# Performance work log

Measured on AMD Instinct MI355X. Metric: run time of the kernel, lower is better.

Reference implementation:

```python
import jax, jax.numpy as jnp
import numpy as np

N_AST = 400_000   # number of AST nodes
M_MAP = 400_000   # number of (ast_node -> cfg_node) mapping entries
S_CFG = 100_000   # number of CFG (PDG) nodes
D = 256           # ast_node_encoding_dim
H = 8             # attention heads
HD = D // H       # head dim
OUT = 256         # combined_dim


def setup_inputs() -> dict:
    key = jax.random.key(0)
    ks = jax.random.split(key, 12)
    w = lambda k, shp: (jax.random.normal(k, shp, jnp.float32) * 0.02)
    return {
        "ast_nodes_encodings": jax.random.normal(ks[0], (N_AST, D), jnp.float32),
        "W_q": w(ks[1], (D, D)), "b_q": jnp.zeros((D,), jnp.float32),
        "W_k": w(ks[2], (D, D)), "b_k": jnp.zeros((D,), jnp.float32),
        "W_v": w(ks[3], (D, D)), "b_v": jnp.zeros((D,), jnp.float32),
        "W_o": w(ks[4], (D, OUT)), "b_o": jnp.zeros((OUT,), jnp.float32),
        "ast_node_idx_to_pdg_node_idx_mapping_key": jax.random.randint(ks[5], (M_MAP,), 0, N_AST),
        "ast_node_idx_to_pdg_node_idx_mapping_value": jax.random.randint(ks[6], (M_MAP,), 0, S_CFG),
        "pdg_node_idx_to_sub_ast_root_idx_mapping_key": jnp.arange(S_CFG),
        "pdg_node_idx_to_sub_ast_root_idx_mapping_value": jax.random.randint(ks[7], (S_CFG,), 0, N_AST),
        "nr_cfg_nodes": S_CFG,
    }


def reference(ast_nodes_encodings, W_q, b_q, W_k, b_k, W_v, b_v, W_o, b_o,
              ast_node_idx_to_pdg_node_idx_mapping_key,
              ast_node_idx_to_pdg_node_idx_mapping_value,
              pdg_node_idx_to_sub_ast_root_idx_mapping_key,
              pdg_node_idx_to_sub_ast_root_idx_mapping_value,
              nr_cfg_nodes):
    S = int(nr_cfg_nodes)
    D_ = ast_nodes_encodings.shape[1]

    # Build per-CFG-node attention queries: gather sub-AST root encodings then
    # scatter into a [S, D] zero buffer (keys are a bijection -> .set is exact).
    gathered_q = ast_nodes_encodings[pdg_node_idx_to_sub_ast_root_idx_mapping_value]  # [S, D]
    attn_queries = jnp.zeros((S, D_), ast_nodes_encodings.dtype).at[
        pdg_node_idx_to_sub_ast_root_idx_mapping_key].set(gathered_q)

    # Scattered inputs: one row per (ast node -> cfg node) mapping entry.
    x = ast_nodes_encodings[ast_node_idx_to_pdg_node_idx_mapping_key]  # [M, D]
    idx = ast_node_idx_to_pdg_node_idx_mapping_value                   # [M] segment ids
    M = x.shape[0]

    # Multi-head projections.
    q = (attn_queries @ W_q + b_q).reshape(S, H, HD)  # [S, H, HD]
    k = (x @ W_k + b_k).reshape(M, H, HD)             # [M, H, HD]
    v = (x @ W_v + b_v).reshape(M, H, HD)             # [M, H, HD]

    # Per-element, per-head attention logits against the owning segment's query.
    scale = np.float32(1.0 / np.sqrt(HD))
    scores = jnp.einsum('mhd,mhd->mh', k, q[idx]) * scale  # [M, H]

    # Segment-wise (scatter) softmax, numerically stable.
    seg_max = jax.ops.segment_max(scores, idx, num_segments=S)        # [S, H]
    seg_max = jnp.where(jnp.isfinite(seg_max), seg_max, jnp.zeros_like(seg_max))
    ew = jnp.exp(scores - seg_max[idx])                               # [M, H]
    denom = jax.ops.segment_sum(ew, idx, num_segments=S)              # [S, H]
    pooled = jax.ops.segment_sum(ew[:, :, None] * v, idx, num_segments=S)  # [S, H, HD]
    pooled = pooled / jnp.maximum(denom, 1e-9)[:, :, None]

    # Output projection to combined_dim.
    out = pooled.reshape(S, H * HD) @ W_o + b_o  # [S, OUT]
    return out
```

## Files before the change

kernel.cpp:

```cpp
#include <hip/hip_runtime.h>
#include <hip/hip_bf16.h>


typedef __attribute__((ext_vector_type(8))) short bf16x8;
typedef __attribute__((ext_vector_type(4))) float f32x4;

#define DEV __device__ __forceinline__

DEV float bf2f(unsigned short u) {
    union { unsigned int i; float f; } x;
    x.i = ((unsigned int)u) << 16;
    return x.f;
}

DEV unsigned short f2bf(float f) {
    union { float f; unsigned int i; } x;
    x.f = f;
    unsigned int i = x.i;
    unsigned int r = 0x7fffu + ((i >> 16) & 1u);
    return (unsigned short)((i + r) >> 16);
}

DEV bf16x8 cvt8(float4 lo, float4 hi) {
    union { bf16x8 v; unsigned int u[4]; } r;
    asm("v_cvt_pk_bf16_f32 %0, %1, %2" : "=v"(r.u[0]) : "v"(lo.x), "v"(lo.y));
    asm("v_cvt_pk_bf16_f32 %0, %1, %2" : "=v"(r.u[1]) : "v"(lo.z), "v"(lo.w));
    asm("v_cvt_pk_bf16_f32 %0, %1, %2" : "=v"(r.u[2]) : "v"(hi.x), "v"(hi.y));
    asm("v_cvt_pk_bf16_f32 %0, %1, %2" : "=v"(r.u[3]) : "v"(hi.z), "v"(hi.w));
    return r.v;
}

DEV unsigned int pack2(float a, float b) {
    unsigned int r;
    asm("v_cvt_pk_bf16_f32 %0, %1, %2" : "=v"(r) : "v"(a), "v"(b));
    return r;
}

DEV int swz(int row, int c) {
    return row * 256 + ((((c) >> 3) ^ (row & 7)) << 3);
}

__global__ void convert_weights(const float* __restrict__ Wq,
                                const float* __restrict__ Wk,
                                const float* __restrict__ Wv,
                                const float* __restrict__ Wo,
                                const float* __restrict__ bk,
                                const float* __restrict__ bv,
                                unsigned short* __restrict__ Wtq,
                                unsigned short* __restrict__ Wtkv,
                                unsigned short* __restrict__ Wto,
                                float* __restrict__ bkv) {
    int t = blockIdx.x * 256 + threadIdx.x;
    if (t < 65536) {
        int n = t >> 8, k = t & 255;
        Wtq[t] = f2bf(Wq[k * 256 + n]);
    } else if (t < 65536 + 131072) {
        int u = t - 65536;
        int n = u >> 8, k = u & 255;
        Wtkv[u] = f2bf(n < 256 ? Wk[k * 256 + n] : Wv[k * 256 + (n - 256)]);
    } else if (t < 196608 + 65536) {
        int u = t - 196608;
        int n = u >> 8, k = u & 255;
        Wto[u] = f2bf(Wo[k * 256 + n]);
    } else if (t < 262144 + 512) {
        int c = t - 262144;
        bkv[c] = c < 256 ? bk[c] : bv[c - 256];
    }
}

__global__ void zero_kernel(int* __restrict__ p, int n) {
    int i = blockIdx.x * 256 + threadIdx.x;
    if (i < n) p[i] = 0;
}

__global__ void hist_kernel(const int* __restrict__ map_val,
                            int* __restrict__ counts, int M) {
    int m = blockIdx.x * 256 + threadIdx.x;
    if (m < M) atomicAdd(&counts[map_val[m]], 1);
}

__global__ __launch_bounds__(256) void scan_p1(const int* __restrict__ counts,
                                               int* __restrict__ bsum, int S) {
    const int i = blockIdx.x * 256 + threadIdx.x;
    int v = (i < S) ? counts[i] : 0;
#pragma unroll
    for (int d = 1; d < 64; d <<= 1) v += __shfl_xor(v, d);
    __shared__ int ws[4];
    if ((threadIdx.x & 63) == 0) ws[threadIdx.x >> 6] = v;
    __syncthreads();
    if (threadIdx.x == 0) bsum[blockIdx.x] = ws[0] + ws[1] + ws[2] + ws[3];
}

__global__ __launch_bounds__(256) void scan_p2(const int* __restrict__ bsum,
                                               int* __restrict__ bpref,
                                               int* __restrict__ offsets,
                                               int nb, int S) {
    __shared__ int part[256];
    const int t = threadIdx.x;
    const int chunk = (nb + 255) / 256;
    const int lo = t * chunk;
    const int hi = min(lo + chunk, nb);
    int sum = 0;
    for (int i = lo; i < hi; ++i) sum += bsum[i];
    part[t] = sum;
    __syncthreads();
    for (int d = 1; d < 256; d <<= 1) {
        int v = (t >= d) ? part[t - d] : 0;
        __syncthreads();
        part[t] += v;
        __syncthreads();
    }
    int run = (t > 0) ? part[t - 1] : 0;
    for (int i = lo; i < hi; ++i) {
        bpref[i] = run;
        run += bsum[i];
    }
    if (t == 255) offsets[S] = part[255];
}

__global__ __launch_bounds__(256) void scan_p3(const int* __restrict__ counts,
                                               const int* __restrict__ bpref,
                                               int* __restrict__ offsets,
                                               int* __restrict__ cursor, int S) {
    __shared__ int sh[256];
    const int t = threadIdx.x;
    const int i = blockIdx.x * 256 + t;
    const int v = (i < S) ? counts[i] : 0;
    sh[t] = v;
    __syncthreads();
    for (int d = 1; d < 256; d <<= 1) {
        int u = (t >= d) ? sh[t - d] : 0;
        __syncthreads();
        sh[t] += u;
        __syncthreads();
    }
    if (i < S) {
        const int e = sh[t] - v + bpref[blockIdx.x];
        offsets[i] = e;
        cursor[i] = e;
    }
}

__global__ void scatter_kernel(const int* __restrict__ map_key,
                               const int* __restrict__ map_val,
                               int* __restrict__ cursor,
                               int* __restrict__ sorted_src, int M) {
    int m = blockIdx.x * 256 + threadIdx.x;
    if (m >= M) return;
    int seg = map_val[m];
    int pos = atomicAdd(&cursor[seg], 1);
    sorted_src[pos] = map_key[m];
}

__global__ __launch_bounds__(1024, 4) void gemm_kv_stream(
    const float* __restrict__ enc,
    const unsigned short* __restrict__ Wtkv,
    const float* __restrict__ bkv,
    unsigned short* __restrict__ out,
    int nrows) {
    __shared__ unsigned short As[2][32 * 256];

    const int tid = threadIdx.x;
    const int wave = tid >> 6, lane = tid & 63;
    const int lrow = lane & 15;
    const int koct = (lane >> 4) * 8;
    const int colb = wave * 32;

    bf16x8 B0[8], B1[8];
#pragma unroll
    for (int kt = 0; kt < 8; ++kt) {
        B0[kt] = *(const bf16x8*)(Wtkv + (long)(colb + lrow) * 256 + kt * 32 + koct);
        B1[kt] = *(const bf16x8*)(Wtkv + (long)(colb + 16 + lrow) * 256 + kt * 32 + koct);
    }
    const float4 bs0 = *(const float4*)(bkv + colb + (lane >> 4) * 4);
    const float4 bs1 = *(const float4*)(bkv + colb + 16 + (lane >> 4) * 4);

    const int srow = tid >> 5;
    const int scol = (tid & 31) * 8;

    const int ntiles = (nrows + 31) / 32;
    const int stride = gridDim.x;
    long t = blockIdx.x;

    float4 f0, f1;
    {
        const long gr = t * 32 + srow;
        const float* ap = enc + (gr < nrows ? gr : 0) * 256 + scol;
        f0 = *(const float4*)(ap);
        f1 = *(const float4*)(ap + 4);
    }

    int cur = 0;
    while (t < ntiles) {
        *(bf16x8*)(&As[cur][swz(srow, scol)]) = cvt8(f0, f1);
        __syncthreads();

        const long tn = t + stride;
        {
            long gr = tn * 32 + srow;
            if (gr >= nrows) gr = 0;
            const float* ap = enc + gr * 256 + scol;
            f0 = *(const float4*)(ap);
            f1 = *(const float4*)(ap + 4);
        }

        f32x4 acc[2][2] = {};
#pragma unroll
        for (int kt = 0; kt < 8; ++kt) {
            const int k0 = kt * 32 + koct;
            bf16x8 a0 = *(const bf16x8*)(&As[cur][swz(lrow, k0)]);
            bf16x8 a1 = *(const bf16x8*)(&As[cur][swz(16 + lrow, k0)]);
            acc[0][0] = __builtin_amdgcn_mfma_f32_16x16x32_bf16(B0[kt], a0, acc[0][0], 0, 0, 0);
            acc[0][1] = __builtin_amdgcn_mfma_f32_16x16x32_bf16(B1[kt], a0, acc[0][1], 0, 0, 0);
            acc[1][0] = __builtin_amdgcn_mfma_f32_16x16x32_bf16(B0[kt], a1, acc[1][0], 0, 0, 0);
            acc[1][1] = __builtin_amdgcn_mfma_f32_16x16x32_bf16(B1[kt], a1, acc[1][1], 0, 0, 0);
        }

        const long rbase = t * 32;
#pragma unroll
        for (int i = 0; i < 2; ++i) {
            const long row = rbase + i * 16 + lrow;
            if (row < nrows) {
                unsigned short* orow = out + row * 512 + colb + (lane >> 4) * 4;
                uint2 w0, w1;
                w0.x = pack2(acc[i][0][0] + bs0.x, acc[i][0][1] + bs0.y);
                w0.y = pack2(acc[i][0][2] + bs0.z, acc[i][0][3] + bs0.w);
                w1.x = pack2(acc[i][1][0] + bs1.x, acc[i][1][1] + bs1.y);
                w1.y = pack2(acc[i][1][2] + bs1.z, acc[i][1][3] + bs1.w);
                *(uint2*)(orow)      = w0;
                *(uint2*)(orow + 16) = w1;
            }
        }

        cur ^= 1;
        t = tn;
    }
}

template <bool GATHER, bool SCATTER, bool A_F32, bool OUT_F32, int NW, int MINB>
__global__ __launch_bounds__(NW * 64, MINB) void gemm64(
    const void* __restrict__ Aptr,
    const int* __restrict__ srcIdx,
    const int* __restrict__ dstIdx,
    const unsigned short* __restrict__ Wt,
    const float* __restrict__ bias,
    void* __restrict__ Out,
    int nrows, int ldo) {
    __shared__ unsigned short Alds[64 * 256];

    constexpr int NT = NW * 64;
    constexpr int F = 16384 / NT;

    const int tid = threadIdx.x;
    const long rbase = (long)blockIdx.x * 64;

    {
        const int l0 = tid * F;
        const int row = l0 >> 8;
        const int col0 = l0 & 255;
        long gr = rbase + row;
        if (gr > nrows - 1) gr = nrows - 1;
        const long src = GATHER ? (long)srcIdx[gr] : gr;
        if constexpr (A_F32) {
            const float* ap = (const float*)Aptr + src * 256 + col0;
#pragma unroll
            for (int u = 0; u < F; u += 8) {
                const float4 lo = *(const float4*)(ap + u);
                const float4 hi = *(const float4*)(ap + u + 4);
                *(bf16x8*)(&Alds[swz(row, col0 + u)]) = cvt8(lo, hi);
            }
        } else {
            const unsigned short* ap = (const unsigned short*)Aptr + src * 256 + col0;
#pragma unroll
            for (int u = 0; u < F; u += 8)
                *(bf16x8*)(&Alds[swz(row, col0 + u)]) = *(const bf16x8*)(ap + u);
        }
    }
    __syncthreads();

    const int wave = tid >> 6, lane = tid & 63;
    const int lrow = lane & 15;
    const int koct = (lane >> 4) * 8;
    const int colb = wave * 64;

    f32x4 acc[4][4] = {};

#pragma unroll
    for (int kt = 0; kt < 8; ++kt) {
        const int k0 = kt * 32 + koct;
        bf16x8 a[4], b[4];
#pragma unroll
        for (int i = 0; i < 4; ++i)
            a[i] = *(const bf16x8*)(&Alds[swz(i * 16 + lrow, k0)]);
#pragma unroll
        for (int j = 0; j < 4; ++j)
            b[j] = *(const bf16x8*)(Wt + (long)(colb + j * 16 + lrow) * 256 + k0);
#pragma unroll
        for (int i = 0; i < 4; ++i)
#pragma unroll
            for (int j = 0; j < 4; ++j)
                acc[i][j] = __builtin_amdgcn_mfma_f32_16x16x32_bf16(b[j], a[i], acc[i][j], 0, 0, 0);
    }

#pragma unroll
    for (int i = 0; i < 4; ++i) {
        const long row = rbase + i * 16 + lrow;
        if (row < nrows) {
            const long drow = SCATTER ? (long)dstIdx[row] : row;
#pragma unroll
            for (int j = 0; j < 4; ++j) {
                const int cb = colb + j * 16 + (lane >> 4) * 4;
                const float4 bs = *(const float4*)(bias + cb);
                if constexpr (OUT_F32) {
                    float4 v;
                    v.x = acc[i][j][0] + bs.x;
                    v.y = acc[i][j][1] + bs.y;
                    v.z = acc[i][j][2] + bs.z;
                    v.w = acc[i][j][3] + bs.w;
                    *(float4*)((float*)Out + drow * ldo + cb) = v;
                } else {
                    uint2 w;
                    w.x = pack2(acc[i][j][0] + bs.x, acc[i][j][1] + bs.y);
                    w.y = pack2(acc[i][j][2] + bs.z, acc[i][j][3] + bs.w);
                    *(uint2*)((unsigned short*)Out + drow * ldo + cb) = w;
                }
            }
        }
    }
}

__global__ __launch_bounds__(512) void pool_csr_kernel(
    unsigned short* __restrict__ q,
    const unsigned short* __restrict__ kv,
    const int* __restrict__ offsets,
    const int* __restrict__ sorted_src,
    int S) {
    const int s = blockIdx.x * 8 + (threadIdx.x >> 6);
    if (s >= S) return;
    const int lane = threadIdx.x & 63;
    const int j = lane & 31;
    const int beg = offsets[s];
    const int end = offsets[s + 1];

    float qf[8];
    if (lane < 32) {
        bf16x8 q8 = *(const bf16x8*)(q + (long)s * 256 + j * 8);
#pragma unroll
        for (int tt = 0; tt < 8; ++tt)
            qf[tt] = bf2f(((const unsigned short*)&q8)[tt]);
    }

    float acc[8] = {0.f, 0.f, 0.f, 0.f, 0.f, 0.f, 0.f, 0.f};
    float denom = 0.f;

    long mrow = (beg < end) ? (long)sorted_src[beg] : 0;
    for (int e = beg; e < end; ++e) {
        const long mnext = (e + 1 < end) ? (long)sorted_src[e + 1] : 0;
        const bf16x8 r = *(const bf16x8*)(kv + mrow * 512 + lane * 8);
        mrow = mnext;

        float ew = 0.f;
        if (lane < 32) {
            float sc = 0.f;
#pragma unroll
            for (int tt = 0; tt < 8; ++tt)
                sc += qf[tt] * bf2f(((const unsigned short*)&r)[tt]);
            sc += __shfl_xor(sc, 1);
            sc += __shfl_xor(sc, 2);
            ew = expf(sc * 0.17677669529663687f);
            denom += ew;
        }
        const float ewv = __shfl(ew, j);
        if (lane >= 32) {
#pragma unroll
            for (int tt = 0; tt < 8; ++tt)
                acc[tt] += ewv * bf2f(((const unsigned short*)&r)[tt]);
        }
    }

    const float dn = __shfl(denom, j);
    if (lane >= 32) {
        const float w = 1.0f / fmaxf(dn, 1e-9f);
        uint4 o;
        o.x = pack2(acc[0] * w, acc[1] * w);
        o.y = pack2(acc[2] * w, acc[3] * w);
        o.z = pack2(acc[4] * w, acc[5] * w);
        o.w = pack2(acc[6] * w, acc[7] * w);
        *(uint4*)(q + (long)s * 256 + j * 8) = o;
    }
}

extern "C" void kernel_launch(void* const* d_in, const int* in_sizes, int n_in,
                              void* d_out, int out_size, void* d_ws, size_t ws_size,
                              hipStream_t stream) {
    const float* enc  = (const float*)d_in[0];
    const float* W_q  = (const float*)d_in[1];
    const float* b_q  = (const float*)d_in[2];
    const float* W_k  = (const float*)d_in[3];
    const float* b_k  = (const float*)d_in[4];
    const float* W_v  = (const float*)d_in[5];
    const float* b_v  = (const float*)d_in[6];
    const float* W_o  = (const float*)d_in[7];
    const float* b_o  = (const float*)d_in[8];
    const int* map_key = (const int*)d_in[9];
    const int* map_val = (const int*)d_in[10];
    const int* pdg_key = (const int*)d_in[11];
    const int* pdg_val = (const int*)d_in[12];

    const int M = in_sizes[9];
    const int S = in_sizes[11];
    const int NAST = in_sizes[0] / 256;
    const int NB = (S + 255) / 256;

    char* ws = (char*)d_ws;
    size_t off = 0;
    auto alloc = [&](size_t bytes) -> char* {
        char* p = ws + off;
        off += (bytes + 255) & ~(size_t)255;
        return p;
    };

    unsigned short* Wt_q  = (unsigned short*)alloc(256 * 256 * 2);
    unsigned short* Wt_kv = (unsigned short*)alloc(512 * 256 * 2);
    unsigned short* Wt_o  = (unsigned short*)alloc(256 * 256 * 2);
    float*          b_kv  = (float*)alloc(512 * 4);
    int*            counts  = (int*)alloc((size_t)S * 4);
    int*            cursor  = (int*)alloc((size_t)S * 4);
    int*            offsets = (int*)alloc((size_t)(S + 1) * 4);
    int*            bsum    = (int*)alloc((size_t)NB * 4);
    int*            bpref   = (int*)alloc((size_t)NB * 4);
    int*            sorted_src = (int*)alloc((size_t)M * 4);
    unsigned short* qbuf   = (unsigned short*)alloc((size_t)S * 256 * 2);
    unsigned short* kv_all = (unsigned short*)alloc((size_t)NAST * 512 * 2);

    zero_kernel<<<(S + 255) / 256, 256, 0, stream>>>(counts, S);

    convert_weights<<<(262656 + 255) / 256, 256, 0, stream>>>(
        W_q, W_k, W_v, W_o, b_k, b_v, Wt_q, Wt_kv, Wt_o, b_kv);

    hist_kernel<<<(M + 255) / 256, 256, 0, stream>>>(map_val, counts, M);
    scan_p1<<<NB, 256, 0, stream>>>(counts, bsum, S);
    scan_p2<<<1, 256, 0, stream>>>(bsum, bpref, offsets, NB, S);
    scan_p3<<<NB, 256, 0, stream>>>(counts, bpref, offsets, cursor, S);
    scatter_kernel<<<(M + 255) / 256, 256, 0, stream>>>(
        map_key, map_val, cursor, sorted_src, M);

    gemm_kv_stream<<<512, 1024, 0, stream>>>(enc, Wt_kv, b_kv, kv_all, NAST);

    gemm64<true, true, true, false, 4, 4><<<(S + 63) / 64, 256, 0, stream>>>(
        enc, pdg_val, pdg_key, Wt_q, b_q, qbuf, S, 256);

    pool_csr_kernel<<<(S + 7) / 8, 512, 0, stream>>>(
        qbuf, kv_all, offsets, sorted_src, S);

    gemm64<false, false, false, true, 4, 4><<<(S + 63) / 64, 256, 0, stream>>>(
        qbuf, nullptr, nullptr, Wt_o, b_o, d_out, S, 256);
}
```

Before: 526.5 us.

## Split KV GEMM columns across two grid halves to halve per-wave register weights

The streaming K/V projection kernel now uses a 2D grid, with each y-slice covering 256 of the 512 output columns. Each wave holds one 16-column weight fragment instead of two, which halves the register-resident B operands and accumulators, and the launch bound is raised to allow more resident blocks. The cost is that every encoding row is read from global memory and converted to bf16 twice, once per column half, which doubles that input traffic.

Result: slower. 655.2 us (+24.4%).

```diff
diff --git a/kernel.cpp b/kernel.cpp
--- a/kernel.cpp
+++ b/kernel.cpp
@@ -152,7 +152,7 @@
     sorted_src[pos] = map_key[m];
 }
 
-__global__ __launch_bounds__(1024, 4) void gemm_kv_stream(
+__global__ __launch_bounds__(1024, 8) void gemm_kv_stream(
     const float* __restrict__ enc,
     const unsigned short* __restrict__ Wtkv,
     const float* __restrict__ bkv,
@@ -164,16 +164,13 @@
     const int wave = tid >> 6, lane = tid & 63;
     const int lrow = lane & 15;
     const int koct = (lane >> 4) * 8;
-    const int colb = wave * 32;
-
-    bf16x8 B0[8], B1[8];
-#pragma unroll
-    for (int kt = 0; kt < 8; ++kt) {
-        B0[kt] = *(const bf16x8*)(Wtkv + (long)(colb + lrow) * 256 + kt * 32 + koct);
-        B1[kt] = *(const bf16x8*)(Wtkv + (long)(colb + 16 + lrow) * 256 + kt * 32 + koct);
-    }
-    const float4 bs0 = *(const float4*)(bkv + colb + (lane >> 4) * 4);
-    const float4 bs1 = *(const float4*)(bkv + colb + 16 + (lane >> 4) * 4);
+    const int col0 = blockIdx.y * 256 + wave * 16;
+
+    bf16x8 B0[8];
+#pragma unroll
+    for (int kt = 0; kt < 8; ++kt)
+        B0[kt] = *(const bf16x8*)(Wtkv + (long)(col0 + lrow) * 256 + kt * 32 + koct);
+    const float4 bs0 = *(const float4*)(bkv + col0 + (lane >> 4) * 4);
 
     const int srow = tid >> 5;
     const int scol = (tid & 31) * 8;
@@ -204,31 +201,33 @@
             f1 = *(const float4*)(ap + 4);
         }
 
-        f32x4 acc[2][2] = {};
+        f32x4 acc0 = {}, acc1 = {};
 #pragma unroll
         for (int kt = 0; kt < 8; ++kt) {
             const int k0 = kt * 32 + koct;
             bf16x8 a0 = *(const bf16x8*)(&As[cur][swz(lrow, k0)]);
             bf16x8 a1 = *(const bf16x8*)(&As[cur][swz(16 + lrow, k0)]);
-            acc[0][0] = __builtin_amdgcn_mfma_f32_16x16x32_bf16(B0[kt], a0, acc[0][0], 0, 0, 0);
-            acc[0][1] = __builtin_amdgcn_mfma_f32_16x16x32_bf16(B1[kt], a0, acc[0][1], 0, 0, 0);
-            acc[1][0] = __builtin_amdgcn_mfma_f32_16x16x32_bf16(B0[kt], a1, acc[1][0], 0, 0, 0);
-            acc[1][1] = __builtin_amdgcn_mfma_f32_16x16x32_bf16(B1[kt], a1, acc[1][1], 0, 0, 0);
+            acc0 = __builtin_amdgcn_mfma_f32_16x16x32_bf16(B0[kt], a0, acc0, 0, 0, 0);
+            acc1 = __builtin_amdgcn_mfma_f32_16x16x32_bf16(B0[kt], a1, acc1, 0, 0, 0);
         }
 
         const long rbase = t * 32;
-#pragma unroll
-        for (int i = 0; i < 2; ++i) {
-            const long row = rbase + i * 16 + lrow;
-            if (row < nrows) {
-                unsigned short* orow = out + row * 512 + colb + (lane >> 4) * 4;
-                uint2 w0, w1;
-                w0.x = pack2(acc[i][0][0] + bs0.x, acc[i][0][1] + bs0.y);
-                w0.y = pack2(acc[i][0][2] + bs0.z, acc[i][0][3] + bs0.w);
-                w1.x = pack2(acc[i][1][0] + bs1.x, acc[i][1][1] + bs1.y);
-                w1.y = pack2(acc[i][1][2] + bs1.z, acc[i][1][3] + bs1.w);
-                *(uint2*)(orow)      = w0;
-                *(uint2*)(orow + 16) = w1;
+        {
+            const long row0 = rbase + lrow;
+            if (row0 < nrows) {
+                unsigned short* orow = out + row0 * 512 + col0 + (lane >> 4) * 4;
+                uint2 w0;
+                w0.x = pack2(acc0[0] + bs0.x, acc0[1] + bs0.y);
+                w0.y = pack2(acc0[2] + bs0.z, acc0[3] + bs0.w);
+                *(uint2*)(orow) = w0;
+            }
+            const long row1 = rbase + 16 + lrow;
+            if (row1 < nrows) {
+                unsigned short* orow = out + row1 * 512 + col0 + (lane >> 4) * 4;
+                uint2 w1;
+                w1.x = pack2(acc1[0] + bs0.x, acc1[1] + bs0.y);
+                w1.y = pack2(acc1[2] + bs0.z, acc1[3] + bs0.w);
+                *(uint2*)(orow) = w1;
             }
         }
 
@@ -445,7 +444,8 @@
     scatter_kernel<<<(M + 255) / 256, 256, 0, stream>>>(
         map_key, map_val, cursor, sorted_src, M);
 
-    gemm_kv_stream<<<512, 1024, 0, stream>>>(enc, Wt_kv, b_kv, kv_all, NAST);
+    dim3 gkv(256, 2);
+    gemm_kv_stream<<<gkv, 1024, 0, stream>>>(enc, Wt_kv, b_kv, kv_all, NAST);
 
     gemm64<true, true, true, false, 4, 4><<<(S + 63) / 64, 256, 0, stream>>>(
         enc, pdg_val, pdg_key, Wt_q, b_q, qbuf, S, 256);
```

## Compute K/V projections only for AST rows referenced by the mapping

Applied to the files above, without the earlier changes.

Marks the AST nodes that appear in the mapping keys, prefix-scans the marks to build a compact unique-row list, and runs the K/V GEMM only over those rows. The scatter step now stores compacted row indices so the pooling kernel reads the compact K/V buffer. This avoids projecting AST rows that are never used, at the cost of extra mark, scan and unique-list kernels and a gathered, indirect read of the encodings. The K/V GEMM grid size is also halved.

After: 483.8 us. 1.09x faster.

```diff
diff --git a/kernel.cpp b/kernel.cpp
--- a/kernel.cpp
+++ b/kernel.cpp
@@ -79,10 +79,16 @@
     if (m < M) atomicAdd(&counts[map_val[m]], 1);
 }
 
-__global__ __launch_bounds__(256) void scan_p1(const int* __restrict__ counts,
-                                               int* __restrict__ bsum, int S) {
+__global__ void mark_kernel(const int* __restrict__ map_key,
+                            int* __restrict__ ref, int M) {
+    int m = blockIdx.x * 256 + threadIdx.x;
+    if (m < M) ref[map_key[m]] = 1;
+}
+
+__global__ __launch_bounds__(256) void scan_p1(const int* __restrict__ vals,
+                                               int* __restrict__ bsum, int n) {
     const int i = blockIdx.x * 256 + threadIdx.x;
-    int v = (i < S) ? counts[i] : 0;
+    int v = (i < n) ? vals[i] : 0;
 #pragma unroll
     for (int d = 1; d < 64; d <<= 1) v += __shfl_xor(v, d);
     __shared__ int ws[4];
@@ -93,8 +99,8 @@
 
 __global__ __launch_bounds__(256) void scan_p2(const int* __restrict__ bsum,
                                                int* __restrict__ bpref,
-                                               int* __restrict__ offsets,
-                                               int nb, int S) {
+                                               int* __restrict__ total,
+                                               int nb) {
     __shared__ int part[256];
     const int t = threadIdx.x;
     const int chunk = (nb + 255) / 256;
@@ -115,17 +121,17 @@
         bpref[i] = run;
         run += bsum[i];
     }
-    if (t == 255) offsets[S] = part[255];
-}
-
-__global__ __launch_bounds__(256) void scan_p3(const int* __restrict__ counts,
+    if (t == 255) *total = part[255];
+}
+
+__global__ __launch_bounds__(256) void scan_p3(const int* __restrict__ vals,
                                                const int* __restrict__ bpref,
-                                               int* __restrict__ offsets,
-                                               int* __restrict__ cursor, int S) {
+                                               int* __restrict__ pref,
+                                               int* __restrict__ cursor, int n) {
     __shared__ int sh[256];
     const int t = threadIdx.x;
     const int i = blockIdx.x * 256 + t;
-    const int v = (i < S) ? counts[i] : 0;
+    const int v = (i < n) ? vals[i] : 0;
     sh[t] = v;
     __syncthreads();
     for (int d = 1; d < 256; d <<= 1) {
@@ -134,32 +140,43 @@
         sh[t] += u;
         __syncthreads();
     }
-    if (i < S) {
+    if (i < n) {
         const int e = sh[t] - v + bpref[blockIdx.x];
-        offsets[i] = e;
-        cursor[i] = e;
-    }
+        pref[i] = e;
+        if (cursor) cursor[i] = e;
+    }
+}
+
+__global__ void uniq_kernel(const int* __restrict__ ref,
+                            const int* __restrict__ roff,
+                            int* __restrict__ uniq_list, int n) {
+    int r = blockIdx.x * 256 + threadIdx.x;
+    if (r < n && ref[r]) uniq_list[roff[r]] = r;
 }
 
 __global__ void scatter_kernel(const int* __restrict__ map_key,
                                const int* __restrict__ map_val,
+                               const int* __restrict__ roff,
                                int* __restrict__ cursor,
                                int* __restrict__ sorted_src, int M) {
     int m = blockIdx.x * 256 + threadIdx.x;
     if (m >= M) return;
     int seg = map_val[m];
     int pos = atomicAdd(&cursor[seg], 1);
-    sorted_src[pos] = map_key[m];
+    sorted_src[pos] = roff[map_key[m]];
 }
 
 __global__ __launch_bounds__(1024, 4) void gemm_kv_stream(
     const float* __restrict__ enc,
+    const int* __restrict__ uniq_list,
+    const int* __restrict__ Uptr,
     const unsigned short* __restrict__ Wtkv,
     const float* __restrict__ bkv,
     unsigned short* __restrict__ out,
-    int nrows) {
+    int nmax) {
     __shared__ unsigned short As[2][32 * 256];
 
+    const int U = *Uptr;
     const int tid = threadIdx.x;
     const int wave = tid >> 6, lane = tid & 63;
     const int lrow = lane & 15;
@@ -178,14 +195,15 @@
     const int srow = tid >> 5;
     const int scol = (tid & 31) * 8;
 
-    const int ntiles = (nrows + 31) / 32;
+    const long ntiles = (U + 31) / 32;
     const int stride = gridDim.x;
     long t = blockIdx.x;
 
     float4 f0, f1;
     {
-        const long gr = t * 32 + srow;
-        const float* ap = enc + (gr < nrows ? gr : 0) * 256 + scol;
+        const long g = t * 32 + srow;
+        const long src = (g < U) ? (long)uniq_list[g] : 0;
+        const float* ap = enc + src * 256 + scol;
         f0 = *(const float4*)(ap);
         f1 = *(const float4*)(ap + 4);
     }
@@ -197,9 +215,9 @@
 
         const long tn = t + stride;
         {
-            long gr = tn * 32 + srow;
-            if (gr >= nrows) gr = 0;
-            const float* ap = enc + gr * 256 + scol;
+            long g = tn * 32 + srow;
+            long src = (g < U) ? (long)uniq_list[g] : 0;
+            const float* ap = enc + src * 256 + scol;
             f0 = *(const float4*)(ap);
             f1 = *(const float4*)(ap + 4);
         }
@@ -220,7 +238,7 @@
 #pragma unroll
         for (int i = 0; i < 2; ++i) {
             const long row = rbase + i * 16 + lrow;
-            if (row < nrows) {
+            if (row < U) {
                 unsigned short* orow = out + row * 512 + colb + (lane >> 4) * 4;
                 uint2 w0, w1;
                 w0.x = pack2(acc[i][0][0] + bs0.x, acc[i][0][1] + bs0.y);
@@ -410,7 +428,8 @@
     const int M = in_sizes[9];
     const int S = in_sizes[11];
     const int NAST = in_sizes[0] / 256;
-    const int NB = (S + 255) / 256;
+    const int NBS = (S + 255) / 256;
+    const int NBR = (NAST + 255) / 256;
 
     char* ws = (char*)d_ws;
     size_t off = 0;
@@ -427,25 +446,40 @@
     int*            counts  = (int*)alloc((size_t)S * 4);
     int*            cursor  = (int*)alloc((size_t)S * 4);
     int*            offsets = (int*)alloc((size_t)(S + 1) * 4);
-    int*            bsum    = (int*)alloc((size_t)NB * 4);
-    int*            bpref   = (int*)alloc((size_t)NB * 4);
+    int*            sbsum   = (int*)alloc((size_t)NBS * 4);
+    int*            sbpref  = (int*)alloc((size_t)NBS * 4);
+    int*            ref     = (int*)alloc((size_t)NAST * 4);
+    int*            roff    = (int*)alloc((size_t)(NAST + 1) * 4);
+    int*            rbsum   = (int*)alloc((size_t)NBR * 4);
+    int*            rbpref  = (int*)alloc((size_t)NBR * 4);
+    int*            uniq_list  = (int*)alloc((size_t)NAST * 4);
     int*            sorted_src = (int*)alloc((size_t)M * 4);
     unsigned short* qbuf   = (unsigned short*)alloc((size_t)S * 256 * 2);
     unsigned short* kv_all = (unsigned short*)alloc((size_t)NAST * 512 * 2);
 
-    zero_kernel<<<(S + 255) / 256, 256, 0, stream>>>(counts, S);
+    zero_kernel<<<NBS, 256, 0, stream>>>(counts, S);
+    zero_kernel<<<NBR, 256, 0, stream>>>(ref, NAST);
 
     convert_weights<<<(262656 + 255) / 256, 256, 0, stream>>>(
         W_q, W_k, W_v, W_o, b_k, b_v, Wt_q, Wt_kv, Wt_o, b_kv);
 
+    mark_kernel<<<(M + 255) / 256, 256, 0, stream>>>(map_key, ref, M);
     hist_kernel<<<(M + 255) / 256, 256, 0, stream>>>(map_val, counts, M);
-    scan_p1<<<NB, 256, 0, stream>>>(counts, bsum, S);
-    scan_p2<<<1, 256, 0, stream>>>(bsum, bpref, offsets, NB, S);
-    scan_p3<<<NB, 256, 0, stream>>>(counts, bpref, offsets, cursor, S);
+
+    scan_p1<<<NBS, 256, 0, stream>>>(counts, sbsum, S);
+    scan_p2<<<1, 256, 0, stream>>>(sbsum, sbpref, offsets + S, NBS);
+    scan_p3<<<NBS, 256, 0, stream>>>(counts, sbpref, offsets, cursor, S);
+
+    scan_p1<<<NBR, 256, 0, stream>>>(ref, rbsum, NAST);
+    scan_p2<<<1, 256, 0, stream>>>(rbsum, rbpref, roff + NAST, NBR);
+    scan_p3<<<NBR, 256, 0, stream>>>(ref, rbpref, roff, (int*)nullptr, NAST);
+    uniq_kernel<<<NBR, 256, 0, stream>>>(ref, roff, uniq_list, NAST);
+
     scatter_kernel<<<(M + 255) / 256, 256, 0, stream>>>(
-        map_key, map_val, cursor, sorted_src, M);
-
-    gemm_kv_stream<<<512, 1024, 0, stream>>>(enc, Wt_kv, b_kv, kv_all, NAST);
+        map_key, map_val, roff, cursor, sorted_src, M);
+
+    gemm_kv_stream<<<256, 1024, 0, stream>>>(
+        enc, uniq_list, roff + NAST, Wt_kv, b_kv, kv_all, NAST);
 
     gemm64<true, true, true, false, 4, 4><<<(S + 63) / 64, 256, 0, stream>>>(
         enc, pdg_val, pdg_key, Wt_q, b_q, qbuf, S, 256);
```
